# Kernel optimization log

Measured on AMD Instinct MI355X. Metric: run time of the kernel, lower is better.

## Reference

```python
import jax, jax.numpy as jnp
import numpy as np

AGENT_TYPE_VEHICLE = 1
AGENT_TYPE_PEDESTRIAN = 2
N_VEHICLE_INTENTIONS = 6
N_PEDESTRIAN_INTENTIONS = 2
INTENTION_LOGIT_DIM = 6


def setup_inputs() -> dict:
    key = jax.random.key(0)
    ks = jax.random.split(key, 10)
    B, N, D = 32, 2048, 512
    H = D // 2
    s_in = 1.0 / np.sqrt(D)
    s_h = 1.0 / np.sqrt(H)
    return {
        "repr3": jax.random.normal(ks[0], (B, N, D), dtype=jnp.float32),
        "agent_type_ids": jax.random.randint(ks[1], (B, N), 0, 4, dtype=jnp.int64),
        # vehicle head: Linear(D, D//2) -> GELU -> Linear(D//2, 6)
        "vW1": jax.random.normal(ks[2], (H, D), dtype=jnp.float32) * s_in,
        "vb1": jax.random.normal(ks[3], (H,), dtype=jnp.float32) * s_in,
        "vW2": jax.random.normal(ks[4], (N_VEHICLE_INTENTIONS, H), dtype=jnp.float32) * s_h,
        "vb2": jax.random.normal(ks[5], (N_VEHICLE_INTENTIONS,), dtype=jnp.float32) * s_h,
        # pedestrian head: Linear(D, D//2) -> GELU -> Linear(D//2, 2)
        "pW1": jax.random.normal(ks[6], (H, D), dtype=jnp.float32) * s_in,
        "pb1": jax.random.normal(ks[7], (H,), dtype=jnp.float32) * s_in,
        "pW2": jax.random.normal(ks[8], (N_PEDESTRIAN_INTENTIONS, H), dtype=jnp.float32) * s_h,
        "pb2": jax.random.normal(ks[9], (N_PEDESTRIAN_INTENTIONS,), dtype=jnp.float32) * s_h,
    }


def _mlp(x, W1, b1, W2, b2):
    # x: [B,N,D] -> [B,N,out]; exact (erf) GELU matches torch nn.GELU()
    h = jax.nn.gelu(jnp.einsum("bnd,hd->bnh", x, W1) + b1, approximate=False)
    return jnp.einsum("bnh,oh->bno", h, W2) + b2


def reference(repr3, agent_type_ids, vW1, vb1, vW2, vb2, pW1, pb1, pW2, pb2):
    v_mask = agent_type_ids == AGENT_TYPE_VEHICLE  # [B,N]
    p_mask = agent_type_ids == AGENT_TYPE_PEDESTRIAN
    v_logits = _mlp(repr3, vW1, vb1, vW2, vb2)  # [B,N,6]
    p_logits = _mlp(repr3, pW1, pb1, pW2, pb2)  # [B,N,2]
    pad = INTENTION_LOGIT_DIM - N_PEDESTRIAN_INTENTIONS
    p_padded = jnp.pad(p_logits, ((0, 0), (0, 0), (0, pad)))  # [B,N,6]
    zero = jnp.zeros((), dtype=repr3.dtype)
    intention_logits = (
        jnp.where(v_mask[..., None], v_logits, zero)
        + jnp.where(p_mask[..., None], p_padded, zero)
    )
    return intention_logits, v_mask, p_mask
```

## Files before the change

### kernel.cpp

```cpp
#include <hip/hip_runtime.h>
#include <hip/hip_bf16.h>
#include <math.h>


#define TOKENS 65536
#define DIM    512
#define HID    256
#define ASTR   40
#define HSTR   264

using short8 = __attribute__((ext_vector_type(8))) short;
using f32x4  = __attribute__((ext_vector_type(4))) float;

__device__ __forceinline__ unsigned int pkrne(float a, float b) {
    unsigned int ua = __float_as_uint(a);
    unsigned int ub = __float_as_uint(b);
    ua += 0x7FFFu + ((ua >> 16) & 1u);
    ub += 0x7FFFu + ((ub >> 16) & 1u);
    return __builtin_amdgcn_perm(ub, ua, 0x07060302u);
}

__device__ __forceinline__ uint2 cvt4(f32x4 v) {
    return make_uint2(pkrne(v[0], v[1]), pkrne(v[2], v[3]));
}

__device__ __forceinline__ __hip_bfloat16 bf16rne(float x) {
    unsigned int u = __float_as_uint(x);
    u += 0x7FFFu + ((u >> 16) & 1u);
    unsigned short hs = (unsigned short)(u >> 16);
    return *(__hip_bfloat16*)&hs;
}

__device__ __forceinline__ float gelu_exact(float x) {
    return 0.5f * x * (1.0f + erff(x * 0.7071067811865475f));
}

__global__ __launch_bounds__(256)
void prep_kernel(const float* __restrict__ vW1, const float* __restrict__ pW1,
                 const float* __restrict__ vW2, const float* __restrict__ pW2,
                 __hip_bfloat16* __restrict__ Wc, __hip_bfloat16* __restrict__ W2c)
{
    const int i = blockIdx.x * 256 + threadIdx.x;
    if (i < 65536) {
        const int flat = i * 4;
        f32x4 v = (flat < 131072) ? *(const f32x4*)(vW1 + flat)
                                  : *(const f32x4*)(pW1 + flat - 131072);
        *(uint2*)(Wc + flat) = cvt4(v);
    } else if (i < 65536 + 2048) {
        const int flat = (i - 65536) * 4;
        const int row = flat >> 8, col = flat & 255;
        f32x4 v = (f32x4){0.f, 0.f, 0.f, 0.f};
        if (row < 6)                      v = *(const f32x4*)(vW2 + row * HID + col);
        else if (row >= 16 && row < 18)   v = *(const f32x4*)(pW2 + (row - 16) * HID + col);
        *(uint2*)(W2c + flat) = cvt4(v);
    }
}

__global__ __launch_bounds__(256, 3)
void intention_heads_kernel(const float* __restrict__ X,
                            const int* __restrict__ ids,
                            const __hip_bfloat16* __restrict__ Wc,
                            const __hip_bfloat16* __restrict__ W2c,
                            const float* __restrict__ vb1,
                            const float* __restrict__ pb1,
                            const float* __restrict__ vb2,
                            const float* __restrict__ pb2,
                            float* __restrict__ out)
{
    __shared__ __align__(16) unsigned char smem[64 * HSTR * 2];
    __hip_bfloat16* A0 = (__hip_bfloat16*)smem;
    __hip_bfloat16* A1 = (__hip_bfloat16*)(smem + 64 * ASTR * 2);
    __hip_bfloat16* H  = (__hip_bfloat16*)smem;

    const int bx   = blockIdx.x;
    const int head = bx & 1;
    const int row0 = (bx >> 1) * 64;

    const int tid  = threadIdx.x;
    const int wave = tid >> 6;
    const int lane = tid & 63;
    const int quad = lane >> 4;
    const int l16  = lane & 15;
    const int wcol = wave * 64;

    const int q  = tid & 7;
    const int r2 = tid >> 3;
    const float* Xs = X + (long)(row0 + r2) * DIM + q * 4;

    const __hip_bfloat16* Wrow[4];
    #pragma unroll
    for (int j = 0; j < 4; ++j)
        Wrow[j] = Wc + (long)(head * 256 + wcol + j * 16 + l16) * DIM + quad * 8;

    f32x4 acc[4][4];
    #pragma unroll
    for (int i = 0; i < 4; ++i)
        #pragma unroll
        for (int j = 0; j < 4; ++j)
            acc[i][j] = (f32x4){0.f, 0.f, 0.f, 0.f};

    {
        f32x4 pa0 = *(const f32x4*)(Xs);
        f32x4 pa1 = *(const f32x4*)(Xs + 32 * DIM);
        *(uint2*)&A0[r2 * ASTR + q * 4]        = cvt4(pa0);
        *(uint2*)&A0[(r2 + 32) * ASTR + q * 4] = cvt4(pa1);
    }
    short8 bcur[4];
    #pragma unroll
    for (int j = 0; j < 4; ++j)
        bcur[j] = *(const short8*)Wrow[j];
    __syncthreads();

    int p = 0;
    for (int it = 0; it < DIM / 32; ++it) {
        __hip_bfloat16* cur = p ? A1 : A0;
        __hip_bfloat16* nxt = p ? A0 : A1;

        short8 af[4];
        #pragma unroll
        for (int i = 0; i < 4; ++i)
            af[i] = *(const short8*)&cur[(i * 16 + l16) * ASTR + quad * 8];

        f32x4 na0, na1;
        short8 bnext[4];
        if (it < 15) {
            na0 = *(const f32x4*)(Xs + (it + 1) * 32);
            na1 = *(const f32x4*)(Xs + 32 * DIM + (it + 1) * 32);
            #pragma unroll
            for (int j = 0; j < 4; ++j)
                bnext[j] = *(const short8*)(Wrow[j] + (it + 1) * 32);
        }

        #pragma unroll
        for (int i = 0; i < 4; ++i)
            #pragma unroll
            for (int j = 0; j < 4; ++j)
                acc[i][j] = __builtin_amdgcn_mfma_f32_16x16x32_bf16(af[i], bcur[j], acc[i][j], 0, 0, 0);

        if (it < 15) {
            *(uint2*)&nxt[r2 * ASTR + q * 4]        = cvt4(na0);
            *(uint2*)&nxt[(r2 + 32) * ASTR + q * 4] = cvt4(na1);
            #pragma unroll
            for (int j = 0; j < 4; ++j)
                bcur[j] = bnext[j];
        }
        __syncthreads();
        p ^= 1;
    }

    const float* b1 = head ? pb1 : vb1;
    float b1v[4];
    #pragma unroll
    for (int j = 0; j < 4; ++j)
        b1v[j] = b1[wcol + j * 16 + l16];

    #pragma unroll
    for (int i = 0; i < 4; ++i) {
        #pragma unroll
        for (int j = 0; j < 4; ++j) {
            const int col = wcol + j * 16 + l16;
            #pragma unroll
            for (int rr = 0; rr < 4; ++rr) {
                const int row = i * 16 + quad * 4 + rr;
                H[row * HSTR + col] = bf16rne(gelu_exact(acc[i][j][rr] + b1v[j]));
            }
        }
    }
    __syncthreads();

    const float* b2 = head ? pb2 : vb2;
    const int nOut = head ? 2 : 6;

    f32x4 acc2 = (f32x4){0.f, 0.f, 0.f, 0.f};
    const int tokb = wave * 16;
    const short* hbase  = (const short*)&H[(tokb + l16) * HSTR + quad * 8];
    const __hip_bfloat16* w2base = W2c + (head * 16 + l16) * HID + quad * 8;
    #pragma unroll
    for (int k0 = 0; k0 < HID; k0 += 32) {
        short8 af    = *(const short8*)(hbase + k0);
        short8 bfrag = *(const short8*)(w2base + k0);
        acc2 = __builtin_amdgcn_mfma_f32_16x16x32_bf16(af, bfrag, acc2, 0, 0, 0);
    }

    const float b2v = (l16 < nOut) ? b2[l16] : 0.0f;

    #pragma unroll
    for (int rr = 0; rr < 4; ++rr) {
        const int t = row0 + tokb + quad * 4 + rr;
        const int type = ids[t];
        if (head == 0) {
            if (l16 == 0) {
                out[TOKENS * 6 + t] = (type == 1) ? 1.0f : 0.0f;
                out[TOKENS * 7 + t] = (type == 2) ? 1.0f : 0.0f;
            }
            if (l16 < 6) {
                if (type == 1)
                    out[t * 6 + l16] = acc2[rr] + b2v;
                else if (type != 2)
                    out[t * 6 + l16] = 0.0f;
            }
        } else {
            if (l16 < 6 && type == 2)
                out[t * 6 + l16] = (l16 < 2) ? (acc2[rr] + b2v) : 0.0f;
        }
    }
}

extern "C" void kernel_launch(void* const* d_in, const int* in_sizes, int n_in,
                              void* d_out, int out_size, void* d_ws, size_t ws_size,
                              hipStream_t stream) {
    (void)n_in; (void)out_size; (void)ws_size;
    const float* X   = (const float*)d_in[0];
    const int*   ids = (const int*)d_in[1];
    const float* vW1 = (const float*)d_in[2];
    const float* vb1 = (const float*)d_in[3];
    const float* vW2 = (const float*)d_in[4];
    const float* vb2 = (const float*)d_in[5];
    const float* pW1 = (const float*)d_in[6];
    const float* pb1 = (const float*)d_in[7];
    const float* pW2 = (const float*)d_in[8];
    const float* pb2 = (const float*)d_in[9];
    float* out = (float*)d_out;

    __hip_bfloat16* Wc  = (__hip_bfloat16*)d_ws;
    __hip_bfloat16* W2c = Wc + 512 * DIM;

    hipLaunchKernelGGL(prep_kernel, dim3(264), dim3(256), 0, stream,
                       vW1, pW1, vW2, pW2, Wc, W2c);

    const int tokens = in_sizes[1];
    const int grid   = (tokens / 64) * 2;

    hipLaunchKernelGGL(intention_heads_kernel, dim3(grid), dim3(256), 0, stream,
                       X, ids, Wc, W2c, vb1, pb1, vb2, pb2, out);
}
```

Before: 280.7 us.

## Compute both heads per block so each X tile is loaded once

```diff
diff --git a/kernel.cpp b/kernel.cpp
--- a/kernel.cpp
+++ b/kernel.cpp
@@ -6,8 +6,8 @@
 #define TOKENS 65536
 #define DIM    512
 #define HID    256
-#define ASTR   40
-#define HSTR   264
+#define ASTR   72
+#define NITER  8
 
 using short8 = __attribute__((ext_vector_type(8))) short;
 using f32x4  = __attribute__((ext_vector_type(4))) float;
@@ -56,7 +56,7 @@
     }
 }
 
-__global__ __launch_bounds__(256, 3)
+__global__ __launch_bounds__(256, 2)
 void intention_heads_kernel(const float* __restrict__ X,
                             const int* __restrict__ ids,
                             const __hip_bfloat16* __restrict__ Wc,
@@ -67,141 +67,170 @@
                             const float* __restrict__ pb2,
                             float* __restrict__ out)
 {
-    __shared__ __align__(16) unsigned char smem[64 * HSTR * 2];
-    __hip_bfloat16* A0 = (__hip_bfloat16*)smem;
-    __hip_bfloat16* A1 = (__hip_bfloat16*)(smem + 64 * ASTR * 2);
-    __hip_bfloat16* H  = (__hip_bfloat16*)smem;
-
-    const int bx   = blockIdx.x;
-    const int head = bx & 1;
-    const int row0 = (bx >> 1) * 64;
-
+    __shared__ __align__(16) unsigned char smem[65536];
+    char* A0 = (char*)smem;
+    char* A1 = (char*)smem + 64 * ASTR * 2;
+
+    const int row0 = blockIdx.x * 64;
     const int tid  = threadIdx.x;
     const int wave = tid >> 6;
     const int lane = tid & 63;
     const int quad = lane >> 4;
     const int l16  = lane & 15;
-    const int wcol = wave * 64;
-
-    const int q  = tid & 7;
-    const int r2 = tid >> 3;
-    const float* Xs = X + (long)(row0 + r2) * DIM + q * 4;
-
-    const __hip_bfloat16* Wrow[4];
-    #pragma unroll
-    for (int j = 0; j < 4; ++j)
-        Wrow[j] = Wc + (long)(head * 256 + wcol + j * 16 + l16) * DIM + quad * 8;
-
-    f32x4 acc[4][4];
+    const int colbase = wave * 128;
+
+    const int srow = tid >> 4;
+    const int scol = tid & 15;
+    const float* Xb = X + (long)(row0 + srow) * DIM + scol * 4;
+    const int wb = srow * (ASTR * 2) + scol * 8;
+
+    const char* Wq = (const char*)Wc;
+    int voff[8];
+    #pragma unroll
+    for (int j = 0; j < 8; ++j)
+        voff[j] = (colbase + j * 16 + l16) * (DIM * 2) + quad * 16;
+
+    const int abase = l16 * (ASTR * 2) + quad * 16;
+
+    f32x4 acc[4][8];
     #pragma unroll
     for (int i = 0; i < 4; ++i)
         #pragma unroll
-        for (int j = 0; j < 4; ++j)
+        for (int j = 0; j < 8; ++j)
             acc[i][j] = (f32x4){0.f, 0.f, 0.f, 0.f};
 
     {
-        f32x4 pa0 = *(const f32x4*)(Xs);
-        f32x4 pa1 = *(const f32x4*)(Xs + 32 * DIM);
-        *(uint2*)&A0[r2 * ASTR + q * 4]        = cvt4(pa0);
-        *(uint2*)&A0[(r2 + 32) * ASTR + q * 4] = cvt4(pa1);
-    }
-    short8 bcur[4];
-    #pragma unroll
-    for (int j = 0; j < 4; ++j)
-        bcur[j] = *(const short8*)Wrow[j];
+        f32x4 x0 = *(const f32x4*)(Xb);
+        f32x4 x1 = *(const f32x4*)(Xb + 16 * DIM);
+        f32x4 x2 = *(const f32x4*)(Xb + 32 * DIM);
+        f32x4 x3 = *(const f32x4*)(Xb + 48 * DIM);
+        *(uint2*)(A0 + wb)            = cvt4(x0);
+        *(uint2*)(A0 + wb + 2304)     = cvt4(x1);
+        *(uint2*)(A0 + wb + 2 * 2304) = cvt4(x2);
+        *(uint2*)(A0 + wb + 3 * 2304) = cvt4(x3);
+    }
+    short8 ba[8];
+    #pragma unroll
+    for (int j = 0; j < 8; ++j)
+        ba[j] = *(const short8*)(Wq + voff[j]);
     __syncthreads();
 
-    int p = 0;
-    for (int it = 0; it < DIM / 32; ++it) {
-        __hip_bfloat16* cur = p ? A1 : A0;
-        __hip_bfloat16* nxt = p ? A0 : A1;
+    #pragma unroll
+    for (int it = 0; it < NITER; ++it) {
+        char* cur = (it & 1) ? A1 : A0;
+        char* nxt = (it & 1) ? A0 : A1;
+
+        short8 bb[8];
+        #pragma unroll
+        for (int j = 0; j < 8; ++j)
+            bb[j] = *(const short8*)(Wq + voff[j] + it * 128 + 64);
+
+        f32x4 n0, n1, n2, n3;
+        if (it < NITER - 1) {
+            const float* Xi = Xb + (it + 1) * 64;
+            n0 = *(const f32x4*)(Xi);
+            n1 = *(const f32x4*)(Xi + 16 * DIM);
+            n2 = *(const f32x4*)(Xi + 32 * DIM);
+            n3 = *(const f32x4*)(Xi + 48 * DIM);
+        }
 
         short8 af[4];
         #pragma unroll
         for (int i = 0; i < 4; ++i)
-            af[i] = *(const short8*)&cur[(i * 16 + l16) * ASTR + quad * 8];
-
-        f32x4 na0, na1;
-        short8 bnext[4];
-        if (it < 15) {
-            na0 = *(const f32x4*)(Xs + (it + 1) * 32);
-            na1 = *(const f32x4*)(Xs + 32 * DIM + (it + 1) * 32);
-            #pragma unroll
-            for (int j = 0; j < 4; ++j)
-                bnext[j] = *(const short8*)(Wrow[j] + (it + 1) * 32);
-        }
-
-        #pragma unroll
-        for (int i = 0; i < 4; ++i)
-            #pragma unroll
-            for (int j = 0; j < 4; ++j)
-                acc[i][j] = __builtin_amdgcn_mfma_f32_16x16x32_bf16(af[i], bcur[j], acc[i][j], 0, 0, 0);
-
-        if (it < 15) {
-            *(uint2*)&nxt[r2 * ASTR + q * 4]        = cvt4(na0);
-            *(uint2*)&nxt[(r2 + 32) * ASTR + q * 4] = cvt4(na1);
-            #pragma unroll
-            for (int j = 0; j < 4; ++j)
-                bcur[j] = bnext[j];
+            af[i] = *(const short8*)(cur + abase + i * 2304);
+        #pragma unroll
+        for (int i = 0; i < 4; ++i)
+            #pragma unroll
+            for (int j = 0; j < 8; ++j)
+                acc[i][j] = __builtin_amdgcn_mfma_f32_16x16x32_bf16(af[i], ba[j], acc[i][j], 0, 0, 0);
+
+        if (it < NITER - 1) {
+            #pragma unroll
+            for (int j = 0; j < 8; ++j)
+                ba[j] = *(const short8*)(Wq + voff[j] + (it + 1) * 128);
+        }
+
+        short8 ag[4];
+        #pragma unroll
+        for (int i = 0; i < 4; ++i)
+            ag[i] = *(const short8*)(cur + abase + i * 2304 + 64);
+        #pragma unroll
+        for (int i = 0; i < 4; ++i)
+            #pragma unroll
+            for (int j = 0; j < 8; ++j)
+                acc[i][j] = __builtin_amdgcn_mfma_f32_16x16x32_bf16(ag[i], bb[j], acc[i][j], 0, 0, 0);
+
+        if (it < NITER - 1) {
+            *(uint2*)(nxt + wb)            = cvt4(n0);
+            *(uint2*)(nxt + wb + 2304)     = cvt4(n1);
+            *(uint2*)(nxt + wb + 2 * 2304) = cvt4(n2);
+            *(uint2*)(nxt + wb + 3 * 2304) = cvt4(n3);
         }
         __syncthreads();
-        p ^= 1;
-    }
-
-    const float* b1 = head ? pb1 : vb1;
-    float b1v[4];
-    #pragma unroll
-    for (int j = 0; j < 4; ++j)
-        b1v[j] = b1[wcol + j * 16 + l16];
+    }
+
+    const float* b1p = (colbase < HID) ? vb1 : pb1;
+    const int cb = colbase & (HID - 1);
+    float b1v[8];
+    #pragma unroll
+    for (int j = 0; j < 8; ++j)
+        b1v[j] = b1p[cb + j * 16 + l16];
 
     #pragma unroll
     for (int i = 0; i < 4; ++i) {
         #pragma unroll
-        for (int j = 0; j < 4; ++j) {
-            const int col = wcol + j * 16 + l16;
+        for (int j = 0; j < 8; ++j) {
+            const int col2 = (colbase + j * 16 + l16) * 2;
             #pragma unroll
             for (int rr = 0; rr < 4; ++rr) {
                 const int row = i * 16 + quad * 4 + rr;
-                H[row * HSTR + col] = bf16rne(gelu_exact(acc[i][j][rr] + b1v[j]));
+                const int byte = ((row << 10) + col2) ^ ((row & 7) << 4);
+                *(__hip_bfloat16*)((char*)smem + byte) =
+                    bf16rne(gelu_exact(acc[i][j][rr] + b1v[j]));
             }
         }
     }
     __syncthreads();
 
-    const float* b2 = head ? pb2 : vb2;
-    const int nOut = head ? 2 : 6;
-
-    f32x4 acc2 = (f32x4){0.f, 0.f, 0.f, 0.f};
     const int tokb = wave * 16;
-    const short* hbase  = (const short*)&H[(tokb + l16) * HSTR + quad * 8];
-    const __hip_bfloat16* w2base = W2c + (head * 16 + l16) * HID + quad * 8;
-    #pragma unroll
-    for (int k0 = 0; k0 < HID; k0 += 32) {
-        short8 af    = *(const short8*)(hbase + k0);
-        short8 bfrag = *(const short8*)(w2base + k0);
-        acc2 = __builtin_amdgcn_mfma_f32_16x16x32_bf16(af, bfrag, acc2, 0, 0, 0);
-    }
-
-    const float b2v = (l16 < nOut) ? b2[l16] : 0.0f;
+    const int rowH = tokb + l16;
+    const int hb   = (rowH << 10) + quad * 16;
+    const int hx   = (rowH & 7) << 4;
+
+    const char* w2v = (const char*)(W2c + l16 * HID) + quad * 16;
+    const char* w2p = (const char*)(W2c + (16 + l16) * HID) + quad * 16;
+
+    f32x4 acc2v = (f32x4){0.f, 0.f, 0.f, 0.f};
+    f32x4 acc2p = (f32x4){0.f, 0.f, 0.f, 0.f};
+    #pragma unroll
+    for (int k = 0; k < 8; ++k) {
+        short8 hv = *(const short8*)((char*)smem + ((hb + k * 64) ^ hx));
+        short8 wv = *(const short8*)(w2v + k * 64);
+        acc2v = __builtin_amdgcn_mfma_f32_16x16x32_bf16(hv, wv, acc2v, 0, 0, 0);
+    }
+    #pragma unroll
+    for (int k = 0; k < 8; ++k) {
+        short8 hp = *(const short8*)((char*)smem + ((hb + 512 + k * 64) ^ hx));
+        short8 wp = *(const short8*)(w2p + k * 64);
+        acc2p = __builtin_amdgcn_mfma_f32_16x16x32_bf16(hp, wp, acc2p, 0, 0, 0);
+    }
+
+    const float b2v = (l16 < 6) ? vb2[l16] : 0.0f;
+    const float b2p = (l16 < 2) ? pb2[l16] : 0.0f;
 
     #pragma unroll
     for (int rr = 0; rr < 4; ++rr) {
         const int t = row0 + tokb + quad * 4 + rr;
         const int type = ids[t];
-        if (head == 0) {
-            if (l16 == 0) {
-                out[TOKENS * 6 + t] = (type == 1) ? 1.0f : 0.0f;
-                out[TOKENS * 7 + t] = (type == 2) ? 1.0f : 0.0f;
-            }
-            if (l16 < 6) {
-                if (type == 1)
-                    out[t * 6 + l16] = acc2[rr] + b2v;
-                else if (type != 2)
-                    out[t * 6 + l16] = 0.0f;
-            }
-        } else {
-            if (l16 < 6 && type == 2)
-                out[t * 6 + l16] = (l16 < 2) ? (acc2[rr] + b2v) : 0.0f;
+        if (l16 == 0) {
+            out[TOKENS * 6 + t] = (type == 1) ? 1.0f : 0.0f;
+            out[TOKENS * 7 + t] = (type == 2) ? 1.0f : 0.0f;
+        }
+        if (l16 < 6) {
+            float v = 0.0f;
+            if (type == 1)                       v = acc2v[rr] + b2v;
+            else if (type == 2 && l16 < 2)       v = acc2p[rr] + b2p;
+            out[t * 6 + l16] = v;
         }
     }
 }
@@ -229,7 +258,7 @@
                        vW1, pW1, vW2, pW2, Wc, W2c);
 
     const int tokens = in_sizes[1];
-    const int grid   = (tokens / 64) * 2;
+    const int grid   = tokens / 64;
 
     hipLaunchKernelGGL(intention_heads_kernel, dim3(grid), dim3(256), 0, stream,
                        X, ids, Wc, W2c, vb1, pb1, vb2, pb2, out);
```

After: 300.9 us. 1.07x slower.

## Stream fp32 X tiles via global_load_lds with swizzle, convert at fragment load

Applied to the files above, without the earlier changes.

```diff
diff --git a/kernel.cpp b/kernel.cpp
--- a/kernel.cpp
+++ b/kernel.cpp
@@ -6,8 +6,8 @@
 #define TOKENS 65536
 #define DIM    512
 #define HID    256
-#define ASTR   40
 #define HSTR   264
+#define NITER  8
 
 using short8 = __attribute__((ext_vector_type(8))) short;
 using f32x4  = __attribute__((ext_vector_type(4))) float;
@@ -68,13 +68,13 @@
                             float* __restrict__ out)
 {
     __shared__ __align__(16) unsigned char smem[64 * HSTR * 2];
-    __hip_bfloat16* A0 = (__hip_bfloat16*)smem;
-    __hip_bfloat16* A1 = (__hip_bfloat16*)(smem + 64 * ASTR * 2);
-    __hip_bfloat16* H  = (__hip_bfloat16*)smem;
-
-    const int bx   = blockIdx.x;
-    const int head = bx & 1;
-    const int row0 = (bx >> 1) * 64;
+    __hip_bfloat16* H = (__hip_bfloat16*)smem;
+
+    const int cpx = gridDim.x >> 3;
+    const int bid = (blockIdx.x & 7) * cpx + (blockIdx.x >> 3);
+
+    const int head = bid & 1;
+    const int row0 = (bid >> 1) * 64;
 
     const int tid  = threadIdx.x;
     const int wave = tid >> 6;
@@ -83,14 +83,14 @@
     const int l16  = lane & 15;
     const int wcol = wave * 64;
 
-    const int q  = tid & 7;
-    const int r2 = tid >> 3;
-    const float* Xs = X + (long)(row0 + r2) * DIM + q * 4;
-
-    const __hip_bfloat16* Wrow[4];
+    const int srowL  = lane >> 4;
+    const int schunk = lane & 15;
+
+    const char* Wq = (const char*)Wc;
+    int boff[4];
     #pragma unroll
     for (int j = 0; j < 4; ++j)
-        Wrow[j] = Wc + (long)(head * 256 + wcol + j * 16 + l16) * DIM + quad * 8;
+        boff[j] = (head * 256 + wcol + j * 16 + l16) * (DIM * 2) + quad * 16;
 
     f32x4 acc[4][4];
     #pragma unroll
@@ -99,54 +99,75 @@
         for (int j = 0; j < 4; ++j)
             acc[i][j] = (f32x4){0.f, 0.f, 0.f, 0.f};
 
-    {
-        f32x4 pa0 = *(const f32x4*)(Xs);
-        f32x4 pa1 = *(const f32x4*)(Xs + 32 * DIM);
-        *(uint2*)&A0[r2 * ASTR + q * 4]        = cvt4(pa0);
-        *(uint2*)&A0[(r2 + 32) * ASTR + q * 4] = cvt4(pa1);
-    }
-    short8 bcur[4];
+    #define STAGE(bufoff, itv)                                               \
+    {                                                                        \
+        _Pragma("unroll")                                                    \
+        for (int u = 0; u < 4; ++u) {                                        \
+            const int seg = wave * 4 + u;                                    \
+            const int row = seg * 4 + srowL;                                 \
+            const int chg = schunk ^ (row & 7);                              \
+            const float* gsrc = X + (long)(row0 + row) * DIM                 \
+                                + (itv) * 64 + chg * 4;                      \
+            __builtin_amdgcn_global_load_lds((const void*)gsrc,              \
+                (void*)(smem + (bufoff) + seg * 1024), 16, 0, 0);            \
+        }                                                                    \
+    }
+
+    STAGE(0, 0);
+    short8 ba[4], bb[4];
     #pragma unroll
     for (int j = 0; j < 4; ++j)
-        bcur[j] = *(const short8*)Wrow[j];
+        ba[j] = *(const short8*)(Wq + boff[j]);
     __syncthreads();
 
-    int p = 0;
-    for (int it = 0; it < DIM / 32; ++it) {
-        __hip_bfloat16* cur = p ? A1 : A0;
-        __hip_bfloat16* nxt = p ? A0 : A1;
-
-        short8 af[4];
-        #pragma unroll
-        for (int i = 0; i < 4; ++i)
-            af[i] = *(const short8*)&cur[(i * 16 + l16) * ASTR + quad * 8];
-
-        f32x4 na0, na1;
-        short8 bnext[4];
-        if (it < 15) {
-            na0 = *(const f32x4*)(Xs + (it + 1) * 32);
-            na1 = *(const f32x4*)(Xs + 32 * DIM + (it + 1) * 32);
+    #pragma unroll 2
+    for (int it = 0; it < NITER; ++it) {
+        const int curo = (it & 1) ? 16384 : 0;
+        const int nxto = (it & 1) ? 0 : 16384;
+
+        if (it < NITER - 1)
+            STAGE(nxto, it + 1);
+        #pragma unroll
+        for (int j = 0; j < 4; ++j)
+            bb[j] = *(const short8*)(Wq + boff[j] + it * 128 + 64);
+
+        #pragma unroll
+        for (int i = 0; i < 4; ++i) {
+            const int row = i * 16 + l16;
+            const int lin = row * 256 + quad * 32;
+            const int sw  = (row & 7) << 4;
+            f32x4 xa = *(const f32x4*)(smem + curo + (lin ^ sw));
+            f32x4 xb = *(const f32x4*)(smem + curo + ((lin + 16) ^ sw));
+            union { short8 s; uint2 u[2]; } f;
+            f.u[0] = cvt4(xa); f.u[1] = cvt4(xb);
             #pragma unroll
             for (int j = 0; j < 4; ++j)
-                bnext[j] = *(const short8*)(Wrow[j] + (it + 1) * 32);
-        }
-
-        #pragma unroll
-        for (int i = 0; i < 4; ++i)
+                acc[i][j] = __builtin_amdgcn_mfma_f32_16x16x32_bf16(f.s, ba[j], acc[i][j], 0, 0, 0);
+        }
+
+        if (it < NITER - 1) {
             #pragma unroll
             for (int j = 0; j < 4; ++j)
-                acc[i][j] = __builtin_amdgcn_mfma_f32_16x16x32_bf16(af[i], bcur[j], acc[i][j], 0, 0, 0);
-
-        if (it < 15) {
-            *(uint2*)&nxt[r2 * ASTR + q * 4]        = cvt4(na0);
-            *(uint2*)&nxt[(r2 + 32) * ASTR + q * 4] = cvt4(na1);
+                ba[j] = *(const short8*)(Wq + boff[j] + (it + 1) * 128);
+        }
+
+        #pragma unroll
+        for (int i = 0; i < 4; ++i) {
+            const int row = i * 16 + l16;
+            const int lin = row * 256 + 128 + quad * 32;
+            const int sw  = (row & 7) << 4;
+            f32x4 xa = *(const f32x4*)(smem + curo + (lin ^ sw));
+            f32x4 xb = *(const f32x4*)(smem + curo + ((lin + 16) ^ sw));
+            union { short8 s; uint2 u[2]; } f;
+            f.u[0] = cvt4(xa); f.u[1] = cvt4(xb);
             #pragma unroll
             for (int j = 0; j < 4; ++j)
-                bcur[j] = bnext[j];
-        }
+                acc[i][j] = __builtin_amdgcn_mfma_f32_16x16x32_bf16(f.s, bb[j], acc[i][j], 0, 0, 0);
+        }
+
         __syncthreads();
-        p ^= 1;
-    }
+    }
+    #undef STAGE
 
     const float* b1 = head ? pb1 : vb1;
     float b1v[4];
```

Result: no change. 282.8 us (+0.7%).

## Deepen X prefetch to two stages with triple-buffered LDS and XCD block remap

Applied to the files above, without the earlier changes.

```diff
diff --git a/kernel.cpp b/kernel.cpp
--- a/kernel.cpp
+++ b/kernel.cpp
@@ -7,6 +7,7 @@
 #define DIM    512
 #define HID    256
 #define ASTR   40
+#define ABUFB  5120
 #define HSTR   264
 
 using short8 = __attribute__((ext_vector_type(8))) short;
@@ -68,13 +69,13 @@
                             float* __restrict__ out)
 {
     __shared__ __align__(16) unsigned char smem[64 * HSTR * 2];
-    __hip_bfloat16* A0 = (__hip_bfloat16*)smem;
-    __hip_bfloat16* A1 = (__hip_bfloat16*)(smem + 64 * ASTR * 2);
-    __hip_bfloat16* H  = (__hip_bfloat16*)smem;
-
-    const int bx   = blockIdx.x;
-    const int head = bx & 1;
-    const int row0 = (bx >> 1) * 64;
+    __hip_bfloat16* H = (__hip_bfloat16*)smem;
+
+    const int cpx = gridDim.x >> 3;
+    const int bid = (blockIdx.x & 7) * cpx + (blockIdx.x >> 3);
+
+    const int head = bid & 1;
+    const int row0 = (bid >> 1) * 64;
 
     const int tid  = threadIdx.x;
     const int wave = tid >> 6;
@@ -99,53 +100,50 @@
         for (int j = 0; j < 4; ++j)
             acc[i][j] = (f32x4){0.f, 0.f, 0.f, 0.f};
 
+    f32x4 ga0 = *(const f32x4*)(Xs);
+    f32x4 ga1 = *(const f32x4*)(Xs + 32 * DIM);
+    f32x4 gb0 = *(const f32x4*)(Xs + 32);
+    f32x4 gb1 = *(const f32x4*)(Xs + 32 * DIM + 32);
     {
-        f32x4 pa0 = *(const f32x4*)(Xs);
-        f32x4 pa1 = *(const f32x4*)(Xs + 32 * DIM);
-        *(uint2*)&A0[r2 * ASTR + q * 4]        = cvt4(pa0);
-        *(uint2*)&A0[(r2 + 32) * ASTR + q * 4] = cvt4(pa1);
-    }
-    short8 bcur[4];
-    #pragma unroll
-    for (int j = 0; j < 4; ++j)
-        bcur[j] = *(const short8*)Wrow[j];
+        __hip_bfloat16* A = (__hip_bfloat16*)smem;
+        *(uint2*)&A[r2 * ASTR + q * 4]        = cvt4(ga0);
+        *(uint2*)&A[(r2 + 32) * ASTR + q * 4] = cvt4(ga1);
+    }
     __syncthreads();
-
-    int p = 0;
+    ga0 = gb0; ga1 = gb1;
+
+    #pragma unroll
     for (int it = 0; it < DIM / 32; ++it) {
-        __hip_bfloat16* cur = p ? A1 : A0;
-        __hip_bfloat16* nxt = p ? A0 : A1;
+        __hip_bfloat16* cur = (__hip_bfloat16*)(smem + (it % 3) * ABUFB);
+        __hip_bfloat16* nxt = (__hip_bfloat16*)(smem + ((it + 1) % 3) * ABUFB);
+
+        if (it < 14) {
+            gb0 = *(const f32x4*)(Xs + (it + 2) * 32);
+            gb1 = *(const f32x4*)(Xs + 32 * DIM + (it + 2) * 32);
+        }
+
+        short8 bc[4];
+        #pragma unroll
+        for (int j = 0; j < 4; ++j)
+            bc[j] = *(const short8*)(Wrow[j] + it * 32);
 
         short8 af[4];
         #pragma unroll
         for (int i = 0; i < 4; ++i)
             af[i] = *(const short8*)&cur[(i * 16 + l16) * ASTR + quad * 8];
-
-        f32x4 na0, na1;
-        short8 bnext[4];
-        if (it < 15) {
-            na0 = *(const f32x4*)(Xs + (it + 1) * 32);
-            na1 = *(const f32x4*)(Xs + 32 * DIM + (it + 1) * 32);
-            #pragma unroll
-            for (int j = 0; j < 4; ++j)
-                bnext[j] = *(const short8*)(Wrow[j] + (it + 1) * 32);
-        }
 
         #pragma unroll
         for (int i = 0; i < 4; ++i)
             #pragma unroll
             for (int j = 0; j < 4; ++j)
-                acc[i][j] = __builtin_amdgcn_mfma_f32_16x16x32_bf16(af[i], bcur[j], acc[i][j], 0, 0, 0);
+                acc[i][j] = __builtin_amdgcn_mfma_f32_16x16x32_bf16(af[i], bc[j], acc[i][j], 0, 0, 0);
 
         if (it < 15) {
-            *(uint2*)&nxt[r2 * ASTR + q * 4]        = cvt4(na0);
-            *(uint2*)&nxt[(r2 + 32) * ASTR + q * 4] = cvt4(na1);
-            #pragma unroll
-            for (int j = 0; j < 4; ++j)
-                bcur[j] = bnext[j];
+            *(uint2*)&nxt[r2 * ASTR + q * 4]        = cvt4(ga0);
+            *(uint2*)&nxt[(r2 + 32) * ASTR + q * 4] = cvt4(ga1);
         }
         __syncthreads();
-        p ^= 1;
+        ga0 = gb0; ga1 = gb1;
     }
 
     const float* b1 = head ? pb1 : vb1;
```

Result: no change. 283.0 us (+0.8%).
